# Kernel tuning notes

Hardware: AMD Instinct MI355X
Metric: run time of the kernel (lower is better)

Reference implementation:

```python
import jax, jax.numpy as jnp
import numpy as np

D = 1024
HEADS = 16
HEAD_DIM = D // HEADS
B = 4
L = 1024


def setup_inputs() -> dict:
    key = jax.random.key(0)
    kq, kk, kv, kw, kb = jax.random.split(key, 5)
    Q = jax.random.normal(kq, (B, L, D), dtype=jnp.float32)
    K = jax.random.normal(kk, (B, L, D), dtype=jnp.float32)
    V = jax.random.normal(kv, (B, L, D), dtype=jnp.float32)
    # Output projection H: torch nn.Linear(D, D) -> weight (D, D), bias (D,)
    lim = 1.0 / np.sqrt(D)
    W_H = jax.random.uniform(kw, (D, D), minval=-lim, maxval=lim, dtype=jnp.float32)
    b_H = jax.random.uniform(kb, (D,), minval=-lim, maxval=lim, dtype=jnp.float32)
    mask = 0  # falsy -> no masking branch, matching `if mask` in the source
    return {"Q": Q, "K": K, "V": V, "W_H": W_H, "b_H": b_H, "mask": mask}


def reference(Q, K, V, W_H, b_H, mask):
    batch, q_len, _ = Q.shape
    k_len = K.shape[1]
    Qh = Q.reshape(batch, q_len, HEADS, HEAD_DIM)
    Kh = K.reshape(batch, k_len, HEADS, HEAD_DIM)
    Vh = V.reshape(batch, k_len, HEADS, HEAD_DIM)
    scores = jnp.einsum('bqhd,bkhd->bhqk', Qh, Kh)  # [B,H,Lq,Lk]
    if mask:  # mask is a Python scalar (0 -> skip), as in source
        scores = jnp.where(mask == 0, -jnp.inf, scores)
    # NOTE: source scales by sqrt(D), not sqrt(head_dim)
    attn = jax.nn.softmax(scores / np.sqrt(D).astype(np.float32), axis=3)
    out = jnp.einsum('bhql,blhd->bqhd', attn, Vh).reshape(batch, q_len, D)
    return out @ W_H.T + b_H
```

## Files before the change

kernel.cpp:

```cpp
#include <hip/hip_runtime.h>
#include <hip/hip_bf16.h>

typedef __attribute__((ext_vector_type(4))) float f32x4;
typedef __attribute__((ext_vector_type(8))) short bf16x8;
typedef __attribute__((ext_vector_type(4))) short bf16x4;

#if __has_builtin(__builtin_amdgcn_mfma_f32_16x16x16_bf16)
#define MFMA_16x16x16(a, b, c) __builtin_amdgcn_mfma_f32_16x16x16_bf16(a, b, c, 0, 0, 0)
#else
#define MFMA_16x16x16(a, b, c) __builtin_amdgcn_mfma_f32_16x16x16bf16_1k(a, b, c, 0, 0, 0)
#endif

constexpr int Bn  = 4;
constexpr int Ln  = 1024;
constexpr int Dn  = 1024;
constexpr int Hn  = 16;
constexpr int HDn = 64;
constexpr int SEGS = Ln / 64;
constexpr int SEG_KV_SHORTS = 8192;

static __device__ __forceinline__ unsigned short bf16r(float f) {
    union { float f; unsigned int u; } x;
    x.f = f;
    unsigned int r = x.u + 0x7fffu + ((x.u >> 16) & 1u);
    return (unsigned short)(r >> 16);
}

__global__ __launch_bounds__(256) void prep_kernel(
    const float* __restrict__ Kg, const float* __restrict__ Vg,
    const float* __restrict__ Wg, unsigned short* __restrict__ KVg,
    unsigned short* __restrict__ Wbf)
{
    const int tid = threadIdx.x;
    if (blockIdx.z == 4) {
        const int r0 = blockIdx.x * 64, c0 = blockIdx.y * 64;
        for (int i = 0; i < 4; ++i) {
            int e4 = i * 256 + tid;
            int r = e4 >> 4, c4 = e4 & 15;
            float4 v = *(const float4*)(Wg + (size_t)(r0 + r) * Dn + c0 + c4 * 4);
            ushort4 o;
            o.x = bf16r(v.x); o.y = bf16r(v.y); o.z = bf16r(v.z); o.w = bf16r(v.w);
            *(ushort4*)(Wbf + (size_t)(r0 + r) * Dn + c0 + c4 * 4) = o;
        }
        return;
    }

    __shared__ unsigned short Tk[64][72];
    __shared__ unsigned short Tv[64][72];
    const int seg = blockIdx.x;
    const int k0  = seg * 64;
    const int h   = blockIdx.y;
    const int b   = blockIdx.z;
    const float* Kb = Kg + (size_t)b * Ln * Dn + h * HDn;
    const float* Vb = Vg + (size_t)b * Ln * Dn + h * HDn;

    for (int i = 0; i < 4; ++i) {
        int e4 = i * 256 + tid;
        int r = e4 >> 4, c4 = e4 & 15;
        float4 kv = *(const float4*)(Kb + (size_t)(k0 + r) * Dn + c4 * 4);
        Tk[r][c4 * 4 + 0] = bf16r(kv.x);
        Tk[r][c4 * 4 + 1] = bf16r(kv.y);
        Tk[r][c4 * 4 + 2] = bf16r(kv.z);
        Tk[r][c4 * 4 + 3] = bf16r(kv.w);
        float4 vv = *(const float4*)(Vb + (size_t)(k0 + r) * Dn + c4 * 4);
        Tv[c4 * 4 + 0][r] = bf16r(vv.x);
        Tv[c4 * 4 + 1][r] = bf16r(vv.y);
        Tv[c4 * 4 + 2][r] = bf16r(vv.z);
        Tv[c4 * 4 + 3][r] = bf16r(vv.w);
    }
    __syncthreads();

    unsigned short* out = KVg + ((size_t)((b * Hn + h) * SEGS + seg)) * SEG_KV_SHORTS;
    for (int i = 0; i < 2; ++i) {
        int s = i * 256 + tid;
        int fid = s >> 6, L = s & 63;
        int l16s = L & 15, qd = L >> 4;
        {
            int n = fid >> 1, half = fid & 1;
            ushort4 lo = *(const ushort4*)&Tk[n * 16 + l16s][half * 32 + qd * 8];
            ushort4 hi = *(const ushort4*)&Tk[n * 16 + l16s][half * 32 + qd * 8 + 4];
            union { ushort4 s[2]; uint4 u; } pk;
            pk.s[0] = lo; pk.s[1] = hi;
            *(uint4*)(out + (size_t)s * 8) = pk.u;
        }
        {
            int dt = fid >> 1, knp = fid & 1;
            ushort4 lo = *(const ushort4*)&Tv[dt * 16 + l16s][knp * 32 + qd * 4];
            ushort4 hi = *(const ushort4*)&Tv[dt * 16 + l16s][knp * 32 + 16 + qd * 4];
            union { ushort4 s[2]; uint4 u; } pk;
            pk.s[0] = lo; pk.s[1] = hi;
            *(uint4*)(out + 4096 + (size_t)s * 8) = pk.u;
        }
    }
}

__global__ __launch_bounds__(256) void attn_kernel(
    const float* __restrict__ Qg, const unsigned short* __restrict__ KVg,
    unsigned short* __restrict__ Xg)
{
    const int tid  = threadIdx.x;
    const int wave = tid >> 6;
    const int lane = tid & 63;
    const int l16  = lane & 15;
    const int quad = lane >> 4;

    const int h  = blockIdx.x;
    const int q0 = blockIdx.y * 128;
    const int b  = blockIdx.z;

    const unsigned short* kvb =
        KVg + (size_t)(b * Hn + h) * SEGS * SEG_KV_SHORTS + (size_t)lane * 8;

    const float SC = 1.4426950408889634f / 32.0f;

    bf16x8 aq[2][2];
    for (int set = 0; set < 2; ++set) {
        const float* qp = Qg + ((size_t)b * Ln + q0 + wave * 32 + set * 16 + l16) * Dn
                             + h * HDn + quad * 8;
        float4 a0 = *(const float4*)qp;
        float4 a1 = *(const float4*)(qp + 4);
        float4 a2 = *(const float4*)(qp + 32);
        float4 a3 = *(const float4*)(qp + 36);
        bf16x8 q0v, q1v;
        q0v[0] = (short)bf16r(a0.x * SC); q0v[1] = (short)bf16r(a0.y * SC);
        q0v[2] = (short)bf16r(a0.z * SC); q0v[3] = (short)bf16r(a0.w * SC);
        q0v[4] = (short)bf16r(a1.x * SC); q0v[5] = (short)bf16r(a1.y * SC);
        q0v[6] = (short)bf16r(a1.z * SC); q0v[7] = (short)bf16r(a1.w * SC);
        q1v[0] = (short)bf16r(a2.x * SC); q1v[1] = (short)bf16r(a2.y * SC);
        q1v[2] = (short)bf16r(a2.z * SC); q1v[3] = (short)bf16r(a2.w * SC);
        q1v[4] = (short)bf16r(a3.x * SC); q1v[5] = (short)bf16r(a3.y * SC);
        q1v[6] = (short)bf16r(a3.z * SC); q1v[7] = (short)bf16r(a3.w * SC);
        aq[set][0] = q0v; aq[set][1] = q1v;
    }

    const bf16x4 ones = (bf16x4){(short)0x3F80, (short)0x3F80,
                                 (short)0x3F80, (short)0x3F80};

    f32x4 Oacc[2][4], Osum[2];
    for (int s = 0; s < 2; ++s) {
        Osum[s] = (f32x4){0.f, 0.f, 0.f, 0.f};
        for (int d = 0; d < 4; ++d) Oacc[s][d] = (f32x4){0.f, 0.f, 0.f, 0.f};
    }

    bf16x8 ka[2][4][2];
    bf16x8 vv[4][2];

    for (int n = 0; n < 4; ++n)
        for (int hf = 0; hf < 2; ++hf)
            ka[0][n][hf] = *(const bf16x8*)(kvb + (n * 2 + hf) * 512);

#pragma unroll
    for (int it = 0; it < SEGS; ++it) {
        const int cur = it & 1, nxt = cur ^ 1;
        const unsigned short* segp = kvb + (size_t)it * SEG_KV_SHORTS;

        for (int dt = 0; dt < 4; ++dt)
            for (int knp = 0; knp < 2; ++knp)
                vv[dt][knp] = *(const bf16x8*)(segp + 4096 + (dt * 2 + knp) * 512);

        for (int n = 0; n < 4; ++n)
            for (int hf = 0; hf < 2; ++hf)
                ka[nxt][n][hf] =
                    *(const bf16x8*)(segp + SEG_KV_SHORTS + (n * 2 + hf) * 512);

        f32x4 st[2][4];
        for (int n = 0; n < 4; ++n) {
            bf16x8 ka0 = ka[cur][n][0], ka1 = ka[cur][n][1];
            for (int set = 0; set < 2; ++set) {
                f32x4 acc = (f32x4){0.f, 0.f, 0.f, 0.f};
                acc = __builtin_amdgcn_mfma_f32_16x16x32_bf16(ka0, aq[set][0], acc, 0, 0, 0);
                acc = __builtin_amdgcn_mfma_f32_16x16x32_bf16(ka1, aq[set][1], acc, 0, 0, 0);
                st[set][n] = acc;
            }
        }

        bf16x4 pf[2][4];
        for (int set = 0; set < 2; ++set)
            for (int n = 0; n < 4; ++n) {
                float p0 = exp2f(st[set][n][0]);
                float p1 = exp2f(st[set][n][1]);
                float p2 = exp2f(st[set][n][2]);
                float p3 = exp2f(st[set][n][3]);
                unsigned int u0 = __float_as_uint(p0) + 0x8000u;
                unsigned int u1 = __float_as_uint(p1) + 0x8000u;
                unsigned int u2 = __float_as_uint(p2) + 0x8000u;
                unsigned int u3 = __float_as_uint(p3) + 0x8000u;
                union { unsigned int u[2]; bf16x4 v; } pk;
                pk.u[0] = __builtin_amdgcn_perm(u1, u0, 0x07060302u);
                pk.u[1] = __builtin_amdgcn_perm(u3, u2, 0x07060302u);
                pf[set][n] = pk.v;
            }

        for (int set = 0; set < 2; ++set)
            for (int kn = 0; kn < 4; ++kn)
                Osum[set] = MFMA_16x16x16(pf[set][kn], ones, Osum[set]);

        for (int dt = 0; dt < 4; ++dt)
            for (int knp = 0; knp < 2; ++knp) {
                bf16x8 v8 = vv[dt][knp];
                bf16x4 lo = __builtin_shufflevector(v8, v8, 0, 1, 2, 3);
                bf16x4 hi = __builtin_shufflevector(v8, v8, 4, 5, 6, 7);
                for (int set = 0; set < 2; ++set) {
                    Oacc[set][dt] = MFMA_16x16x16(pf[set][knp * 2], lo, Oacc[set][dt]);
                    Oacc[set][dt] = MFMA_16x16x16(pf[set][knp * 2 + 1], hi, Oacc[set][dt]);
                }
            }
    }

    unsigned short* Xb = Xg + ((size_t)b * Ln + q0) * Dn + h * HDn;
    for (int set = 0; set < 2; ++set)
        for (int r = 0; r < 4; ++r) {
            float linv = 1.f / Osum[set][r];
            int row = wave * 32 + set * 16 + quad * 4 + r;
            for (int dt = 0; dt < 4; ++dt)
                Xb[(size_t)row * Dn + dt * 16 + l16] =
                    bf16r(Oacc[set][dt][r] * linv);
        }
}

__global__ __launch_bounds__(256) void proj_kernel(
    const unsigned short* __restrict__ Xg, const unsigned short* __restrict__ Wbf,
    const float* __restrict__ bg, float* __restrict__ Yg)
{
    __shared__ unsigned short Xs[128][72];
    __shared__ unsigned short Wsh[64][72];

    const int tid  = threadIdx.x;
    const int wave = tid >> 6;
    const int lane = tid & 63;
    const int l16  = lane & 15;
    const int quad = lane >> 4;
    const int mw   = (wave & 1) * 64;
    const int nw   = (wave >> 1) * 32;

    const int n0 = blockIdx.x * 64;
    const int m0 = blockIdx.y * 128;

    f32x4 acc[4][2];
    for (int mt = 0; mt < 4; ++mt)
        for (int nt = 0; nt < 2; ++nt)
            acc[mt][nt] = (f32x4){0.f, 0.f, 0.f, 0.f};

    for (int it = 0; it < Dn / 64; ++it) {
        const int kk0 = it * 64;
        __syncthreads();
        {
            for (int i = 0; i < 4; ++i) {
                int s = i * 256 + tid;
                int r = s >> 3, c8 = s & 7;
                *(uint4*)&Xs[r][c8 * 8] =
                    *(const uint4*)(Xg + (size_t)(m0 + r) * Dn + kk0 + c8 * 8);
            }
            for (int i = 0; i < 2; ++i) {
                int s = i * 256 + tid;
                int r = s >> 3, c8 = s & 7;
                *(uint4*)&Wsh[r][c8 * 8] =
                    *(const uint4*)(Wbf + (size_t)(n0 + r) * Dn + kk0 + c8 * 8);
            }
        }
        __syncthreads();

        bf16x8 af[4][2], bfr[2][2];
        for (int mt = 0; mt < 4; ++mt)
            for (int kk = 0; kk < 2; ++kk)
                af[mt][kk] = *(const bf16x8*)&Xs[mw + mt * 16 + l16][kk * 32 + quad * 8];
        for (int nt = 0; nt < 2; ++nt)
            for (int kk = 0; kk < 2; ++kk)
                bfr[nt][kk] = *(const bf16x8*)&Wsh[nw + nt * 16 + l16][kk * 32 + quad * 8];
        for (int mt = 0; mt < 4; ++mt)
            for (int nt = 0; nt < 2; ++nt) {
                acc[mt][nt] = __builtin_amdgcn_mfma_f32_16x16x32_bf16(
                    af[mt][0], bfr[nt][0], acc[mt][nt], 0, 0, 0);
                acc[mt][nt] = __builtin_amdgcn_mfma_f32_16x16x32_bf16(
                    af[mt][1], bfr[nt][1], acc[mt][nt], 0, 0, 0);
            }
    }

    for (int nt = 0; nt < 2; ++nt) {
        int col = n0 + nw + nt * 16 + l16;
        float bb = bg[col];
        for (int mt = 0; mt < 4; ++mt)
            for (int r = 0; r < 4; ++r) {
                int row = m0 + mw + mt * 16 + quad * 4 + r;
                Yg[(size_t)row * Dn + col] = acc[mt][nt][r] + bb;
            }
    }
}

extern "C" void kernel_launch(void* const* d_in, const int* in_sizes, int n_in,
                              void* d_out, int out_size, void* d_ws, size_t ws_size,
                              hipStream_t stream) {
    const float* Q    = (const float*)d_in[0];
    const float* K    = (const float*)d_in[1];
    const float* V    = (const float*)d_in[2];
    const float* W    = (const float*)d_in[3];
    const float* bias = (const float*)d_in[4];

    const size_t KV_SHORTS = (size_t)Bn * Hn * SEGS * SEG_KV_SHORTS;
    unsigned short* KV  = (unsigned short*)d_ws;
    unsigned short* Wbf = KV + KV_SHORTS + 16384;
    unsigned short* X   = Wbf + (size_t)Dn * Dn;
    float* Y = (float*)d_out;

    dim3 gp(SEGS, Hn, Bn + 1);
    prep_kernel<<<gp, 256, 0, stream>>>(K, V, W, KV, Wbf);

    dim3 g1(Hn, Ln / 128, Bn);
    attn_kernel<<<g1, 256, 0, stream>>>(Q, KV, X);

    dim3 g2(Dn / 64, (Bn * Ln) / 128);
    proj_kernel<<<g2, 256, 0, stream>>>(X, Wbf, bias, Y);
}
```

Measured before the change: 166.2 us.

## Use direct global-to-LDS loads in projection, tune launch bounds and unrolling

```diff
diff --git a/kernel.cpp b/kernel.cpp
--- a/kernel.cpp
+++ b/kernel.cpp
@@ -24,6 +24,13 @@
     x.f = f;
     unsigned int r = x.u + 0x7fffu + ((x.u >> 16) & 1u);
     return (unsigned short)(r >> 16);
+}
+
+static __device__ __forceinline__ void gll16(const unsigned short* g,
+                                             unsigned short* l) {
+    __builtin_amdgcn_global_load_lds(
+        (const __attribute__((address_space(1))) unsigned int*)g,
+        (__attribute__((address_space(3))) unsigned int*)l, 16, 0, 0);
 }
 
 __global__ __launch_bounds__(256) void prep_kernel(
@@ -94,7 +101,7 @@
     }
 }
 
-__global__ __launch_bounds__(256) void attn_kernel(
+__global__ __launch_bounds__(256, 2) void attn_kernel(
     const float* __restrict__ Qg, const unsigned short* __restrict__ KVg,
     unsigned short* __restrict__ Xg)
 {
@@ -149,7 +156,7 @@
         for (int hf = 0; hf < 2; ++hf)
             ka[0][n][hf] = *(const bf16x8*)(kvb + (n * 2 + hf) * 512);
 
-#pragma unroll
+#pragma unroll 2
     for (int it = 0; it < SEGS; ++it) {
         const int cur = it & 1, nxt = cur ^ 1;
         const unsigned short* segp = kvb + (size_t)it * SEG_KV_SHORTS;
@@ -218,12 +225,12 @@
         }
 }
 
-__global__ __launch_bounds__(256) void proj_kernel(
+__global__ __launch_bounds__(256, 2) void proj_kernel(
     const unsigned short* __restrict__ Xg, const unsigned short* __restrict__ Wbf,
     const float* __restrict__ bg, float* __restrict__ Yg)
 {
-    __shared__ unsigned short Xs[128][72];
-    __shared__ unsigned short Wsh[64][72];
+    __shared__ unsigned short Xs[128 * 64];
+    __shared__ unsigned short Wsh[64 * 64];
 
     const int tid  = threadIdx.x;
     const int wave = tid >> 6;
@@ -233,8 +240,8 @@
     const int mw   = (wave & 1) * 64;
     const int nw   = (wave >> 1) * 32;
 
-    const int n0 = blockIdx.x * 64;
-    const int m0 = blockIdx.y * 128;
+    const int m0 = blockIdx.x * 128;
+    const int n0 = blockIdx.y * 64;
 
     f32x4 acc[4][2];
     for (int mt = 0; mt < 4; ++mt)
@@ -244,29 +251,25 @@
     for (int it = 0; it < Dn / 64; ++it) {
         const int kk0 = it * 64;
         __syncthreads();
-        {
-            for (int i = 0; i < 4; ++i) {
-                int s = i * 256 + tid;
-                int r = s >> 3, c8 = s & 7;
-                *(uint4*)&Xs[r][c8 * 8] =
-                    *(const uint4*)(Xg + (size_t)(m0 + r) * Dn + kk0 + c8 * 8);
-            }
-            for (int i = 0; i < 2; ++i) {
-                int s = i * 256 + tid;
-                int r = s >> 3, c8 = s & 7;
-                *(uint4*)&Wsh[r][c8 * 8] =
-                    *(const uint4*)(Wbf + (size_t)(n0 + r) * Dn + kk0 + c8 * 8);
-            }
+        for (int j = 0; j < 4; ++j) {
+            int c = j * 256 + wave * 64 + lane;
+            gll16(Xg + (size_t)(m0 + (c >> 3)) * Dn + kk0 + (c & 7) * 8,
+                  Xs + (size_t)(j * 256 + wave * 64) * 8);
+        }
+        for (int j = 0; j < 2; ++j) {
+            int c = j * 256 + wave * 64 + lane;
+            gll16(Wbf + (size_t)(n0 + (c >> 3)) * Dn + kk0 + (c & 7) * 8,
+                  Wsh + (size_t)(j * 256 + wave * 64) * 8);
         }
         __syncthreads();
 
         bf16x8 af[4][2], bfr[2][2];
         for (int mt = 0; mt < 4; ++mt)
             for (int kk = 0; kk < 2; ++kk)
-                af[mt][kk] = *(const bf16x8*)&Xs[mw + mt * 16 + l16][kk * 32 + quad * 8];
+                af[mt][kk] = *(const bf16x8*)&Xs[(mw + mt * 16 + l16) * 64 + kk * 32 + quad * 8];
         for (int nt = 0; nt < 2; ++nt)
             for (int kk = 0; kk < 2; ++kk)
-                bfr[nt][kk] = *(const bf16x8*)&Wsh[nw + nt * 16 + l16][kk * 32 + quad * 8];
+                bfr[nt][kk] = *(const bf16x8*)&Wsh[(nw + nt * 16 + l16) * 64 + kk * 32 + quad * 8];
         for (int mt = 0; mt < 4; ++mt)
             for (int nt = 0; nt < 2; ++nt) {
                 acc[mt][nt] = __builtin_amdgcn_mfma_f32_16x16x32_bf16(
@@ -308,6 +311,6 @@
     dim3 g1(Hn, Ln / 128, Bn);
     attn_kernel<<<g1, 256, 0, stream>>>(Q, KV, X);
 
-    dim3 g2(Dn / 64, (Bn * Ln) / 128);
+    dim3 g2((Bn * Ln) / 128, Dn / 64);
     proj_kernel<<<g2, 256, 0, stream>>>(X, Wbf, bias, Y);
 }
```

Result: slower. 170.2 us (+2.4%).
